# Kernel tuning notes

Measured on AMD Instinct MI355X. Metric: run time of the kernel, lower is better.

Reference implementation:

```python
import jax, jax.numpy as jnp
import numpy as np

C = 256          # channels
D = C // 4       # q/k dim and angle-embedding hidden_dim
SIGMA = 15.0
BN_EPS = 1e-5
N_LAYERS = 4


def angle_embed(angles, proj_w, proj_b):
    """AngleEmbedding: sinusoidal PE (detached in torch) + Linear proj.
    angles [...,], returns [..., D]. Interleaved sin/cos matches the torch
    cat([sin,cos],dim=2).view(...) layout."""
    factor = 180.0 / (np.pi * SIGMA)
    idx = angles * factor
    div_term = jnp.exp(jnp.arange(0, D, 2, dtype=jnp.float32) * (-np.log(10000.0) / D))  # [D/2]
    om = idx[..., None] * div_term                                  # [..., D/2]
    emb = jnp.stack([jnp.sin(om), jnp.cos(om)], axis=-1).reshape(*angles.shape, D)
    emb = jax.lax.stop_gradient(emb)  # torch: embeddings.detach()
    return emb @ proj_w.T + proj_b


def sa_layer(x, pca, a_self, a_cross, Wq, Wk, Wv, Wvp, Wl, bl, bn_g, bn_b,
             p1w, p1b, p2w, p2b, beta_x, beta_w, picked):
    # x, pca: [B, C, N]
    xq = jnp.einsum('oc,bcn->bno', Wq, x)              # [B,N,D]  q_conv (tied to k_conv_pca)
    k_lrf = jnp.einsum('oc,bcn->bon', Wk, x)           # [B,D,N]
    k_pca = jnp.einsum('oc,bcn->bon', Wq, pca)         # [B,D,N]  weight-tied to q
    energy_lrf = jnp.einsum('bno,bom->bnm', xq, k_lrf)
    energy_pca = jnp.einsum('bno,bom->bnm', xq, k_pca)
    # relative-angle bias terms
    emb1 = angle_embed(a_self, p1w, p1b)               # [B,N,N,D]
    energy_lrf = energy_lrf + jnp.einsum('bnc,bnmc->bnm', xq, emb1)
    emb2 = angle_embed(a_cross, p2w, p2b)              # [B,N,D]
    energy_pca = energy_pca + jnp.einsum('bnc,bmc->bnm', xq, emb2)
    # learn_weight=True combination, softmax over last dim, then column renorm
    energy = jax.nn.softmax(beta_w * energy_lrf + (1.0 - beta_w) * energy_pca, axis=-1)
    energy = energy / (1e-12 + energy.sum(axis=1, keepdims=True))
    point_relation = energy[:, picked, :][:, None, :]  # [B,1,N]
    x_lrf = jnp.einsum('oc,bcn,bnm->bom', Wv, x, energy)
    x_pca = jnp.einsum('oc,bcn,bnm->bom', Wvp, pca, energy)
    x_r = beta_x * x_lrf + (1.0 - beta_x) * x_pca
    h = jnp.einsum('oc,bcn->bon', Wl, x - x_r) + bl[:, None]
    # BatchNorm1d in eval mode: running_mean=0, running_var=1
    h = h / jnp.sqrt(1.0 + BN_EPS) * bn_g[:, None] + bn_b[:, None]
    return x + jax.nn.gelu(h, approximate=False), point_relation


def forward(lrf, pca, angle_self, angle_cross, Wq, Wk, Wv, Wvp, Wl, bl,
            bn_g, bn_b, p1w, p1b, p2w, p2b, beta_x, beta_w, picked):
    x = lrf
    outs = []
    for i in range(N_LAYERS):
        x, _ = sa_layer(x, pca, angle_self, angle_cross, Wq[i], Wk[i], Wv[i],
                        Wvp[i], Wl[i], bl[i], bn_g[i], bn_b[i], p1w[i], p1b[i],
                        p2w[i], p2b[i], beta_x[i], beta_w[i], picked)
        outs.append(x)
    return jnp.concatenate(outs, axis=1)   # [B, 4*C, N]


def setup_inputs() -> dict:
    key = jax.random.key(0)
    ks = jax.random.split(key, 18)
    B, N, L = 64, 128, N_LAYERS
    s = 0.05
    return {
        'lrf': jax.random.normal(ks[0], (B, C, N), dtype=jnp.float32),
        'pca': jax.random.normal(ks[1], (B, C, N), dtype=jnp.float32),
        'angle_self': jax.random.uniform(ks[2], (B, N, N), dtype=jnp.float32),
        'angle_cross': jax.random.uniform(ks[3], (B, N), dtype=jnp.float32),
        'Wq': jax.random.normal(ks[4], (L, D, C)) * s,
        'Wk': jax.random.normal(ks[5], (L, D, C)) * s,
        'Wv': jax.random.normal(ks[6], (L, C, C)) * s,
        'Wvp': jax.random.normal(ks[7], (L, C, C)) * s,
        'Wl': jax.random.normal(ks[8], (L, C, C)) * s,
        'bl': jax.random.normal(ks[9], (L, C)) * s,
        'bn_g': jnp.ones((L, C), dtype=jnp.float32),
        'bn_b': jnp.zeros((L, C), dtype=jnp.float32),
        'p1w': jax.random.normal(ks[10], (L, D, D)) * s,
        'p1b': jax.random.normal(ks[11], (L, D)) * s,
        'p2w': jax.random.normal(ks[12], (L, D, D)) * s,
        'p2b': jax.random.normal(ks[13], (L, D)) * s,
        'beta_x': jnp.full((L,), 0.6, dtype=jnp.float32),
        'beta_w': jnp.full((L,), 0.6, dtype=jnp.float32),
        'picked': 0,
    }


def reference(lrf, pca, angle_self, angle_cross, Wq, Wk, Wv, Wvp, Wl, bl,
              bn_g, bn_b, p1w, p1b, p2w, p2b, beta_x, beta_w, picked):
    return forward(lrf, pca, angle_self, angle_cross, Wq, Wk, Wv, Wvp, Wl, bl,
                   bn_g, bn_b, p1w, p1b, p2w, p2b, beta_x, beta_w, picked)
```

## Files before the change

kernel.cpp:

```cpp
#include <hip/hip_runtime.h>
#include <cstdint>
#include <cstddef>


#define BB 64
#define CH 256
#define NP 128
#define DQ 64
#define NLAYERS 4

#define ANG_FACTOR 3.8197186342054885f
#define DIV_STEP   0.28782313662425575f

#define LROW 264
#define LROW2 136

typedef unsigned short u16;
typedef __attribute__((ext_vector_type(8))) short sh8;
typedef __attribute__((ext_vector_type(4))) float f32x4;
#define MFMA(a, b, c) __builtin_amdgcn_mfma_f32_16x16x32_bf16(a, b, c, 0, 0, 0)

static __device__ __forceinline__ u16 f2bf(float x) {
  unsigned u = __float_as_uint(x);
  return (u16)((u + 0x7FFFu + ((u >> 16) & 1u)) >> 16);
}
static __device__ __forceinline__ float bf2f(u16 h) {
  return __uint_as_float(((unsigned)h) << 16);
}

__global__ __launch_bounds__(256) void k_init(
    const float* __restrict__ Wv, const float* __restrict__ Wvp,
    const float* __restrict__ Wl, const float* __restrict__ Wq,
    const float* __restrict__ Wk, const float* __restrict__ p1w,
    const float* __restrict__ p2w, const float* __restrict__ pca,
    const float* __restrict__ lrf, const float* __restrict__ ac,
    u16* __restrict__ Wlbf, u16* __restrict__ Wqhi, u16* __restrict__ Wqlo,
    u16* __restrict__ Wkhi, u16* __restrict__ Wklo, u16* __restrict__ p1wT,
    u16* __restrict__ p2wbf, u16* __restrict__ pThi, u16* __restrict__ pTlo,
    u16* __restrict__ xThi, u16* __restrict__ xTlo,
    u16* __restrict__ WvT, u16* __restrict__ WvpT, u16* __restrict__ emb2bf)
{
  __shared__ __align__(16) float tl[64 * 65];
  int blk = blockIdx.x, tid = threadIdx.x;
  if (blk < 256) {
    int i = (blk * 256 + tid) * 4;
    float4 v = *(const float4*)(Wl + i);
    u16 o[4] = {f2bf(v.x), f2bf(v.y), f2bf(v.z), f2bf(v.w)};
    *(uint2*)(Wlbf + i) = *(const uint2*)o;
  } else if (blk < 384) {
    int bb = blk - 256;
    const float* s = (bb < 64) ? Wq : Wk;
    u16* dh = (bb < 64) ? Wqhi : Wkhi;
    u16* dl = (bb < 64) ? Wqlo : Wklo;
    int i = ((bb & 63) * 256 + tid) * 4;
    float4 v = *(const float4*)(s + i);
    float vv[4] = {v.x, v.y, v.z, v.w};
    u16 h[4], l[4];
#pragma unroll
    for (int r = 0; r < 4; r++) {
      h[r] = f2bf(vv[r]);
      l[r] = f2bf(vv[r] - bf2f(h[r]));
    }
    *(uint2*)(dh + i) = *(const uint2*)h;
    *(uint2*)(dl + i) = *(const uint2*)l;
  } else if (blk < 388) {
    int l = blk - 384;
    const float* src = p1w + (size_t)l * DQ * DQ;
    u16* dst = p1wT + (size_t)l * DQ * DQ;
#pragma unroll
    for (int i = 0; i < 16; i++) {
      int idx = tid + i * 256;
      int dd = idx >> 6, oo = idx & 63;
      dst[idx] = f2bf(src[oo * DQ + dd]);
    }
  } else if (blk < 392) {
    int l = blk - 388;
    const float* src = p2w + (size_t)l * DQ * DQ;
    u16* dst = p2wbf + (size_t)l * DQ * DQ;
#pragma unroll
    for (int i = 0; i < 16; i++) {
      int idx = tid + i * 256;
      dst[idx] = f2bf(src[idx]);
    }
  } else if (blk < 1416) {
    int bi = blk - 392;
    int nt = bi & 1, y = (bi >> 1) & 7, b = bi >> 4;
    int ct = y & 3, is_lrf = y >> 2;
    const float* x = is_lrf ? lrf : pca;
    u16* hiT = is_lrf ? xThi : pThi;
    u16* loT = is_lrf ? xTlo : pTlo;
    {
      int col = tid & 63, rq = tid >> 6;
      const float* src = x + (size_t)b * CH * NP + (size_t)(ct * 64) * NP + nt * 64;
#pragma unroll
      for (int i = 0; i < 16; i++) {
        int c = rq + i * 4;
        tl[col * 65 + c] = src[(size_t)c * NP + col];
      }
// ... 119 lines not shown
    u16* WH = WS;
    u16* WL = WS + 32 * LROW;
    {
      const u16* sH = Wqhi + (size_t)l * DQ * CH + (size_t)dt * 32 * CH;
      const u16* sL = Wqlo + (size_t)l * DQ * CH + (size_t)dt * 32 * CH;
      STAGE_W(WH, sH)
      STAGE_W(WL, sL)
    }
    __syncthreads();
    const u16* B0h = pThi + ((size_t)b * NP + nt * 32 + lm) * CH + lk * 8;
    const u16* B1h = B0h + 16 * CH;
    const u16* B0l = pTlo + ((size_t)b * NP + nt * 32 + lm) * CH + lk * 8;
    const u16* B1l = B0l + 16 * CH;
    f32x4 acc[2][2] = {};
#pragma unroll
    for (int kb = 0; kb < 4; kb++) {
      sh8 rb0h[2], rb1h[2], rb0l[2], rb1l[2];
#pragma unroll
      for (int u = 0; u < 2; u++) {
        int o = (kb * 2 + u) * 32;
        rb0h[u] = *(const sh8*)(B0h + o); rb1h[u] = *(const sh8*)(B1h + o);
        rb0l[u] = *(const sh8*)(B0l + o); rb1l[u] = *(const sh8*)(B1l + o);
      }
#pragma unroll
      for (int u = 0; u < 2; u++) {
        int o2 = (kb * 2 + u) * 32 + lk * 8;
        sh8 a0h = *(const sh8*)&WH[lm * LROW + o2];
        sh8 a1h = *(const sh8*)&WH[(16 + lm) * LROW + o2];
        sh8 a0l = *(const sh8*)&WL[lm * LROW + o2];
        sh8 a1l = *(const sh8*)&WL[(16 + lm) * LROW + o2];
        acc[0][0] = MFMA(a0h, rb0h[u], acc[0][0]);
        acc[0][0] = MFMA(a0h, rb0l[u], acc[0][0]);
        acc[0][0] = MFMA(a0l, rb0h[u], acc[0][0]);
        acc[0][1] = MFMA(a0h, rb1h[u], acc[0][1]);
        acc[0][1] = MFMA(a0h, rb1l[u], acc[0][1]);
        acc[0][1] = MFMA(a0l, rb1h[u], acc[0][1]);
        acc[1][0] = MFMA(a1h, rb0h[u], acc[1][0]);
        acc[1][0] = MFMA(a1h, rb0l[u], acc[1][0]);
        acc[1][0] = MFMA(a1l, rb0h[u], acc[1][0]);
        acc[1][1] = MFMA(a1h, rb1h[u], acc[1][1]);
        acc[1][1] = MFMA(a1h, rb1l[u], acc[1][1]);
        acc[1][1] = MFMA(a1l, rb1h[u], acc[1][1]);
      }
    }
    {
      const u16* A20 = p2wbf + (size_t)l * DQ * DQ + ((size_t)(dt * 32) + lm) * DQ + lk * 8;
      const u16* A21 = A20 + 16 * DQ;
      const u16* B20 = emb2bf + ((size_t)b * NP + nt * 32 + lm) * DQ + lk * 8;
      const u16* B21 = B20 + 16 * DQ;
#pragma unroll
      for (int ks = 0; ks < 2; ks++) {
        int o = ks * 32;
        sh8 a0 = *(const sh8*)(A20 + o), a1 = *(const sh8*)(A21 + o);
        sh8 b0 = *(const sh8*)(B20 + o), b1 = *(const sh8*)(B21 + o);
        acc[0][0] = MFMA(a0, b0, acc[0][0]);
        acc[0][1] = MFMA(a0, b1, acc[0][1]);
        acc[1][0] = MFMA(a1, b0, acc[1][0]);
        acc[1][1] = MFMA(a1, b1, acc[1][1]);
      }
    }
#pragma unroll
    for (int i = 0; i < 2; i++)
#pragma unroll
      for (int j = 0; j < 2; j++) {
        int n = nt * 32 + j * 16 + lm;
        int d0 = dt * 32 + i * 16 + lk * 4;
        size_t off = (((size_t)l * BB + b) * NP + n) * DQ + d0;
        f32x4 v = acc[i][j];
        u16 h[4], lo[4];
#pragma unroll
        for (int r2 = 0; r2 < 4; r2++) {
          float vv = v[r2] + p2b[l * DQ + d0 + r2];
          h[r2] = f2bf(vv);
          lo[r2] = f2bf(vv - bf2f(h[r2]));
        }
        *(uint2*)&KP2hiA[off] = *(const uint2*)h;
        *(uint2*)&KP2loA[off] = *(const uint2*)lo;
      }
  } else {
    int bi = blockIdx.x - 512;
    int l = bi >> 9, rest = bi & 511;
    int ct = rest >> 6, b = rest & 63;
    int nt = tid >> 6;
    u16* WH = WS;
    {
      const u16* sH = M2b + (size_t)l * CH * CH + (size_t)ct * 32 * CH;
      STAGE_W(WH, sH)
    }
    __syncthreads();
    const u16* X0 = pThi + ((size_t)b * NP + nt * 32 + lm) * CH + lk * 8;
    const u16* X1 = X0 + 16 * CH;
    f32x4 a00 = {}, a01 = {}, a10 = {}, a11 = {};
#pragma unroll
    for (int kb = 0; kb < 2; kb++) {
      sh8 rx0[4], rx1[4];
#pragma unroll
      for (int u = 0; u < 4; u++) {
        int o = (kb * 4 + u) * 32;
        rx0[u] = *(const sh8*)(X0 + o); rx1[u] = *(const sh8*)(X1 + o);
      }
#pragma unroll
      for (int u = 0; u < 4; u++) {
        int o2 = (kb * 4 + u) * 32 + lk * 8;
        sh8 w0 = *(const sh8*)&WH[lm * LROW + o2];
        sh8 w1 = *(const sh8*)&WH[(16 + lm) * LROW + o2];
        a00 = MFMA(rx0[u], w0, a00);
        a01 = MFMA(rx0[u], w1, a01);
        a10 = MFMA(rx1[u], w0, a10);
        a11 = MFMA(rx1[u], w1, a11);
      }
    }
    f32x4 acc[2][2] = {{a00, a01}, {a10, a11}};
#pragma unroll
    for (int i = 0; i < 2; i++)
#pragma unroll
      for (int j = 0; j < 2; j++) {
        int n0 = nt * 32 + i * 16 + lk * 4;
        int c = ct * 32 + j * 16 + lm;
        u16 ov[4];
#pragma unroll
        for (int r2 = 0; r2 < 4; r2++) ov[r2] = f2bf(acc[i][j][r2]);
        *(uint2*)&WlUPA[(((size_t)l * BB + b) * CH + c) * NP + n0] = *(const uint2*)ov;
      }
  }
}

__global__ __launch_bounds__(256) void k_qu4(
    const u16* __restrict__ xThi, const u16* __restrict__ xTlo,
    const u16* __restrict__ Wqhi, const u16* __restrict__ Wqlo,
    const u16* __restrict__ Wkhi, const u16* __restrict__ Wklo,
    const u16* __restrict__ Mb, const u16* __restrict__ Wlbf,
    const u16* __restrict__ WlUP, u16* __restrict__ XQhi, u16* __restrict__ XQlo,
    u16* __restrict__ KLThi, u16* __restrict__ KLTlo,
    u16* __restrict__ WlU, float* __restrict__ Afp)
{
  __shared__ __align__(16) u16 WS[2 * 32 * LROW];
  int tid = threadIdx.x, lane = tid & 63;
  int lm = lane & 15, lk = lane >> 4;
  if (blockIdx.x < 256) {
    int bi = blockIdx.x;
    int mat = bi >> 7, rest = bi & 127;
    int dt = rest >> 6, b = rest & 63;
    int nt = tid >> 6;
    u16* WH = WS;
    u16* WL = WS + 32 * LROW;
    {
      const u16* sH = (mat ? Wkhi : Wqhi) + (size_t)dt * 32 * CH;
      const u16* sL = (mat ? Wklo : Wqlo) + (size_t)dt * 32 * CH;
      STAGE_W(WH, sH)
      STAGE_W(WL, sL)
    }
    __syncthreads();
    const u16* B0h = xThi + ((size_t)b * NP + nt * 32 + lm) * CH + lk * 8;
    const u16* B1h = B0h + 16 * CH;
    const u16* B0l = xTlo + ((size_t)b * NP + nt * 32 + lm) * CH + lk * 8;
    const u16* B1l = B0l + 16 * CH;
    f32x4 acc[2][2] = {};
#pragma unroll
    for (int kb = 0; kb < 4; kb++) {
      sh8 rb0h[2], rb1h[2], rb0l[2], rb1l[2];
#pragma unroll
      for (int u = 0; u < 2; u++) {
        int o = (kb * 2 + u) * 32;
        rb0h[u] = *(const sh8*)(B0h + o); rb1h[u] = *(const sh8*)(B1h + o);
        rb0l[u] = *(const sh8*)(B0l + o); rb1l[u] = *(const sh8*)(B1l + o);
      }
#pragma unroll
      for (int u = 0; u < 2; u++) {
        int o2 = (kb * 2 + u) * 32 + lk * 8;
        sh8 a0h = *(const sh8*)&WH[lm * LROW + o2];
        sh8 a1h = *(const sh8*)&WH[(16 + lm) * LROW + o2];
        sh8 a0l = *(const sh8*)&WL[lm * LROW + o2];
        sh8 a1l = *(const sh8*)&WL[(16 + lm) * LROW + o2];
        acc[0][0] = MFMA(a0h, rb0h[u], acc[0][0]);
        acc[0][0] = MFMA(a0h, rb0l[u], acc[0][0]);
        acc[0][0] = MFMA(a0l, rb0h[u], acc[0][0]);
        acc[0][1] = MFMA(a0h, rb1h[u], acc[0][1]);
        acc[0][1] = MFMA(a0h, rb1l[u], acc[0][1]);
        acc[0][1] = MFMA(a0l, rb1h[u], acc[0][1]);
        acc[1][0] = MFMA(a1h, rb0h[u], acc[1][0]);
        acc[1][0] = MFMA(a1h, rb0l[u], acc[1][0]);
        acc[1][0] = MFMA(a1l, rb0h[u], acc[1][0]);
        acc[1][1] = MFMA(a1h, rb1h[u], acc[1][1]);
        acc[1][1] = MFMA(a1h, rb1l[u], acc[1][1]);
        acc[1][1] = MFMA(a1l, rb1h[u], acc[1][1]);
      }
    }
#pragma unroll
    for (int i = 0; i < 2; i++)
#pragma unroll
      for (int j = 0; j < 2; j++) {
        int n = nt * 32 + j * 16 + lm;
        int d0 = dt * 32 + i * 16 + lk * 4;
        size_t off = ((size_t)b * NP + n) * DQ + d0;
        f32x4 v = acc[i][j];
        u16 h[4], lo[4];
#pragma unroll
        for (int r2 = 0; r2 < 4; r2++) {
          h[r2] = f2bf(v[r2]);
          lo[r2] = f2bf(v[r2] - bf2f(h[r2]));
        }
        if (mat == 0) {
          *(uint2*)&XQhi[off] = *(const uint2*)h;
          *(uint2*)&XQlo[off] = *(const uint2*)lo;
        } else {
          *(uint2*)&KLThi[off] = *(const uint2*)h;
          *(uint2*)&KLTlo[off] = *(const uint2*)lo;
        }
      }
  } else if (blockIdx.x < 768) {
    int bi = blockIdx.x - 256;
    int ct = bi >> 6, b = bi & 63;
    int nt = tid >> 6;
    u16* WH = WS;
    {
      const u16* sH = Mb + (size_t)ct * 32 * CH;
      STAGE_W(WH, sH)
    }
    __syncthreads();
    const u16* X0 = xThi + ((size_t)b * NP + nt * 32 + lm) * CH + lk * 8;
    const u16* X1 = X0 + 16 * CH;
    f32x4 a00 = {}, a01 = {}, a10 = {}, a11 = {};
#pragma unroll
    for (int kb = 0; kb < 2; kb++) {
      sh8 rx0[4], rx1[4];
#pragma unroll
      for (int u = 0; u < 4; u++) {
        int o = (kb * 4 + u) * 32;
        rx0[u] = *(const sh8*)(X0 + o); rx1[u] = *(const sh8*)(X1 + o);
      }
#pragma unroll
      for (int u = 0; u < 4; u++) {
        int o2 = (kb * 4 + u) * 32 + lk * 8;
        sh8 w0 = *(const sh8*)&WH[lm * LROW + o2];
        sh8 w1 = *(const sh8*)&WH[(16 + lm) * LROW + o2];
        a00 = MFMA(rx0[u], w0, a00);
        a01 = MFMA(rx0[u], w1, a01);
        a10 = MFMA(rx1[u], w0, a10);
        a11 = MFMA(rx1[u], w1, a11);
      }
    }
    f32x4 acc[2][2] = {{a00, a01}, {a10, a11}};
#pragma unroll
    for (int i = 0; i < 2; i++)
#pragma unroll
      for (int j = 0; j < 2; j++) {
        int n0 = nt * 32 + i * 16 + lk * 4;
        int c = ct * 32 + j * 16 + lm;
        size_t off = ((size_t)b * CH + c) * NP + n0;
        uint2 up = *(const uint2*)&WlUP[off];
        const u16* uph = (const u16*)&up;
        u16 ov[4];
#pragma unroll
        for (int r2 = 0; r2 < 4; r2++)
          ov[r2] = f2bf(acc[i][j][r2] + bf2f(uph[r2]));
        *(uint2*)&WlU[off] = *(const uint2*)ov;
      }
  } else {
    int bi = blockIdx.x - 768;
    int ct = bi >> 6, b = bi & 63;
    int nt = tid >> 6;
    u16* WH = WS;
    {
      const u16* sH = Wlbf + (size_t)ct * 32 * CH;
      STAGE_W(WH, sH)
    }
    __syncthreads();
    const u16* X0 = xThi + ((size_t)b * NP + nt * 32 + lm) * CH + lk * 8;
    const u16* X1 = X0 + 16 * CH;
    f32x4 a00 = {}, a01 = {}, a10 = {}, a11 = {};
#pragma unroll
    for (int kb = 0; kb < 2; kb++) {
      sh8 rx0[4], rx1[4];
#pragma unroll
      for (int u = 0; u < 4; u++) {
        int o = (kb * 4 + u) * 32;
        rx0[u] = *(const sh8*)(X0 + o); rx1[u] = *(const sh8*)(X1 + o);
      }
#pragma unroll
      for (int u = 0; u < 4; u++) {
        int o2 = (kb * 4 + u) * 32 + lk * 8;
        sh8 w0 = *(const sh8*)&WH[lm * LROW + o2];
        sh8 w1 = *(const sh8*)&WH[(16 + lm) * LROW + o2];
        a00 = MFMA(rx0[u], w0, a00);
        a01 = MFMA(rx0[u], w1, a01);
        a10 = MFMA(rx1[u], w0, a10);
        a11 = MFMA(rx1[u], w1, a11);
      }
    }
    f32x4 acc[2][2] = {{a00, a01}, {a10, a11}};
#pragma unroll
    for (int i = 0; i < 2; i++)
#pragma unroll
      for (int j = 0; j < 2; j++) {
        int n0 = nt * 32 + i * 16 + lk * 4;
        int c = ct * 32 + j * 16 + lm;
        float4 v = {acc[i][j][0], acc[i][j][1], acc[i][j][2], acc[i][j][3]};
        *(float4*)&Afp[((size_t)b * CH + c) * NP + n0] = v;
      }
  }
}

__global__ __launch_bounds__(256) void k_att(
    const u16* __restrict__ XQhi, const u16* __restrict__ XQlo,
    const u16* __restrict__ KLThi, const u16* __restrict__ KLTlo,
    const u16* __restrict__ KP2hi, const u16* __restrict__ KP2lo,
    const u16* __restrict__ p1wT, const float* __restrict__ p1b,
    const float* __restrict__ AS, const float* __restrict__ beta_w, int layer,
    u16* __restrict__ PT, float* __restrict__ SCLp)
{
  __shared__ __align__(16) char smem[25856];
  int tid = threadIdx.x;
  int lane = tid & 63;
  int lm = lane & 15, lk = lane >> 4;
  int g = blockIdx.x & 3, b = blockIdx.x >> 2;
  int wave = tid >> 6;
  float* q1sh = (float*)smem;
  float* c1sh = q1sh + 32 * 66;
  float* divs = c1sh + 32;
  float* Esh  = divs + 32;
  if (tid < 32) divs[tid] = __expf(-(float)tid * DIV_STEP);
  float bw = beta_w[layer], obw = 1.0f - bw;
  {
    int mt = wave;
    size_t arow = ((size_t)b * NP + mt * 32 + lm) * DQ + lk * 8;
    size_t brow = ((size_t)b * NP + g * 32 + lm) * DQ + lk * 8;
    const u16* L0h = KLThi + arow;
    const u16* L0l = KLTlo + arow;
    const u16* P0h = KP2hi + arow;
    const u16* P0l = KP2lo + arow;
    const u16* X0h = XQhi + brow;
    const u16* X0l = XQlo + brow;
    sh8 xh[2][2], xl[2][2], lh[2][2], llr[2][2], ph[2][2], pl[2][2];
#pragma unroll
    for (int row = 0; row < 2; row++) {
#pragma unroll
      for (int ks = 0; ks < 2; ks++) {
        int o = row * 16 * DQ + ks * 32;
        xh[row][ks] = *(const sh8*)(X0h + o);
        xl[row][ks] = *(const sh8*)(X0l + o);
        lh[row][ks] = *(const sh8*)(L0h + o);
        llr[row][ks] = *(const sh8*)(L0l + o);
        ph[row][ks] = *(const sh8*)(P0h + o);
        pl[row][ks] = *(const sh8*)(P0l + o);
      }
    }
    f32x4 aL[2][2] = {};
    f32x4 aP[2][2] = {};
#pragma unroll
    for (int ks = 0; ks < 2; ks++) {
#pragma unroll
      for (int i = 0; i < 2; i++) {
#pragma unroll
        for (int j = 0; j < 2; j++) {
          aL[i][j] = MFMA(lh[i][ks], xh[j][ks], aL[i][j]);
          aL[i][j] = MFMA(lh[i][ks], xl[j][ks], aL[i][j]);
          aL[i][j] = MFMA(llr[i][ks], xh[j][ks], aL[i][j]);
          aP[i][j] = MFMA(ph[i][ks], xh[j][ks], aP[i][j]);
          aP[i][j] = MFMA(ph[i][ks], xl[j][ks], aP[i][j]);
          aP[i][j] = MFMA(pl[i][ks], xh[j][ks], aP[i][j]);
        }
      }
    }
#pragma unroll
    for (int i = 0; i < 2; i++)
#pragma unroll
      for (int j = 0; j < 2; j++) {
        int nloc = j * 16 + lm;
        int mloc = mt * 32 + i * 16 + lk * 4;
        float4 v;
        v.x = bw * aL[i][j][0] + obw * aP[i][j][0];
        v.y = bw * aL[i][j][1] + obw * aP[i][j][1];
        v.z = bw * aL[i][j][2] + obw * aP[i][j][2];
        v.w = bw * aL[i][j][3] + obw * aP[i][j][3];
        *(float4*)&Esh[nloc * 132 + mloc] = v;
      }
  }
  if (wave < 2) {
    const u16* A0 = XQhi + ((size_t)b * NP + g * 32 + lm) * DQ + lk * 8;
    const u16* A1 = A0 + 16 * DQ;
    const u16* B0 = p1wT + ((size_t)(wave * 32) + lm) * DQ + lk * 8;
    const u16* B1 = B0 + 16 * DQ;
    f32x4 q[2][2] = {};
// ... 20 lines not shown
    const u16* xs = XQhi + ((size_t)b * NP + g * 32 + n) * DQ + o0;
    uint2 w0 = *(const uint2*)xs;
    uint2 w1 = *(const uint2*)(xs + 4);
    const u16* hh = (const u16*)&w0;
    const u16* h2 = (const u16*)&w1;
    float s = 0.0f;
#pragma unroll
    for (int k = 0; k < 4; k++) s = fmaf(bf2f(hh[k]), p1b[o0 + k], s);
#pragma unroll
    for (int k = 0; k < 4; k++) s = fmaf(bf2f(h2[k]), p1b[o0 + 4 + k], s);
    s += __shfl_xor(s, 1);
    s += __shfl_xor(s, 2);
    s += __shfl_xor(s, 4);
    if ((tid & 7) == 0) c1sh[n] = s;
  }
  __syncthreads();
  {
    int n = tid >> 3, mc = (tid & 7) * 16;
    size_t asrow = ((size_t)b * NP + g * 32 + n) * NP + mc;
    float idxv[16], bias[16];
    float c1v = c1sh[n];
#pragma unroll
    for (int k4 = 0; k4 < 4; k4++) {
      float4 a4 = *(const float4*)&AS[asrow + k4 * 4];
      idxv[k4 * 4 + 0] = a4.x * ANG_FACTOR;
      idxv[k4 * 4 + 1] = a4.y * ANG_FACTOR;
      idxv[k4 * 4 + 2] = a4.z * ANG_FACTOR;
      idxv[k4 * 4 + 3] = a4.w * ANG_FACTOR;
    }
#pragma unroll
    for (int k = 0; k < 16; k++) bias[k] = c1v;
    for (int j = 0; j < 32; j++) {
      float dv = divs[j];
      float qs = q1sh[n * 66 + 2 * j], qc = q1sh[n * 66 + 2 * j + 1];
#pragma unroll
      for (int k = 0; k < 16; k++) {
        float s, c;
        __sincosf(idxv[k] * dv, &s, &c);
        bias[k] = fmaf(qs, s, bias[k]);
        bias[k] = fmaf(qc, c, bias[k]);
      }
    }
    float ev[16], mx = -1e30f;
#pragma unroll
    for (int k = 0; k < 16; k++) {
      ev[k] = Esh[n * 132 + mc + k] + bw * bias[k];
      mx = fmaxf(mx, ev[k]);
    }
    mx = fmaxf(mx, __shfl_xor(mx, 1));
    mx = fmaxf(mx, __shfl_xor(mx, 2));
    mx = fmaxf(mx, __shfl_xor(mx, 4));
    float s = 0.0f;
#pragma unroll
    for (int k = 0; k < 16; k++) {
      ev[k] = __expf(ev[k] - mx);
      s += ev[k];
    }
    s += __shfl_xor(s, 1);
    s += __shfl_xor(s, 2);
    s += __shfl_xor(s, 4);
    float inv = 1.0f / s;
#pragma unroll
    for (int k = 0; k < 16; k++) Esh[n * 132 + mc + k] = ev[k] * inv;
  }
  __syncthreads();
  {
    int m = tid >> 1, nc = (tid & 1) * 16;
    float s = 0.0f;
    u16 tmp[16];
#pragma unroll
    for (int k = 0; k < 16; k++) {
      float v = Esh[(nc + k) * 132 + m];
      s += v;
      tmp[k] = f2bf(v);
    }
    u16* dst = PT + ((size_t)b * NP + m) * NP + g * 32 + nc;
    *(uint4*)&dst[0] = *(const uint4*)&tmp[0];
    *(uint4*)&dst[8] = *(const uint4*)&tmp[8];
    s += __shfl_xor(s, 1);
    if ((tid & 1) == 0) SCLp[((size_t)b * 4 + g) * NP + m] = s;
  }
}

__global__ __launch_bounds__(256) void k_h3(
    const u16* __restrict__ WlU, const u16* __restrict__ PT,
    const float* __restrict__ SCLp, const float* __restrict__ Afp,
    const float* __restrict__ bl, const float* __restrict__ bng,
    const float* __restrict__ bnb, const float* __restrict__ xsrc, int xbs,
    float* __restrict__ out, int layer,
    u16* __restrict__ xThi_o, u16* __restrict__ xTlo_o)
{
  int bi = blockIdx.x;
  int ct = bi >> 6, b = bi & 63;
  int tid = threadIdx.x, lane = tid & 63, nt = tid >> 6;
  int lm = lane & 15, lk = lane >> 4;
  __shared__ __align__(16) u16 WS2[32 * LROW2];
  {
    const u16* src = WlU + ((size_t)b * CH + ct * 32) * NP;
#pragma unroll
    for (int it = 0; it < 2; it++) {
      int idx = tid + it * 256, row = idx >> 4, chq = idx & 15;
      *(uint4*)&WS2[row * LROW2 + chq * 8] = *(const uint4*)(src + row * NP + chq * 8);
    }
  }
  __syncthreads();
  const u16* B0 = PT + ((size_t)b * NP + nt * 32 + lm) * NP + lk * 8;
  const u16* B1 = B0 + 16 * NP;
  sh8 rB0[4], rB1[4];
#pragma unroll
  for (int ks = 0; ks < 4; ks++) {
    int o = ks * 32;
    rB0[ks] = *(const sh8*)(B0 + o);
    rB1[ks] = *(const sh8*)(B1 + o);
  }
  f32x4 a00 = {}, a01 = {}, a10 = {}, a11 = {};
#pragma unroll
  for (int ks = 0; ks < 4; ks++) {
    int o2 = ks * 32 + lk * 8;
    sh8 w0 = *(const sh8*)&WS2[lm * LROW2 + o2];
    sh8 w1 = *(const sh8*)&WS2[(16 + lm) * LROW2 + o2];
    a00 = MFMA(w0, rB0[ks], a00);
    a01 = MFMA(w0, rB1[ks], a01);
    a10 = MFMA(w1, rB0[ks], a10);
    a11 = MFMA(w1, rB1[ks], a11);
  }
  f32x4 acc[2][2] = {{a00, a01}, {a10, a11}};
  const float rbn = 0.999995000037499687f;
#pragma unroll
  for (int i = 0; i < 2; i++)
#pragma unroll
    for (int j = 0; j < 2; j++) {
      int m = nt * 32 + j * 16 + lm;
      int cq = ct * 32 + i * 16 + lk * 4;
      const float* sp = SCLp + (size_t)b * 4 * NP + m;
      float scl = 1.0f / (1e-12f + sp[0] + sp[NP] + sp[2 * NP] + sp[3 * NP]);
      u16 hh[4], llv[4];
#pragma unroll
      for (int r = 0; r < 4; r++) {
        int c = cq + r;
        float a = Afp[((size_t)b * CH + c) * NP + m];
        float h = a - acc[i][j][r] * scl + bl[c];
        h = h * rbn * bng[c] + bnb[c];
        float gg = 0.5f * h * (1.0f + erff(h * 0.70710678118654752440f));
        float ov = xsrc[(size_t)b * xbs + (size_t)c * NP + m] + gg;
        out[((size_t)b * 4 * CH + (size_t)layer * CH + c) * NP + m] = ov;
        hh[r] = f2bf(ov);
        llv[r] = f2bf(ov - bf2f(hh[r]));
      }
      size_t xoff = ((size_t)b * NP + m) * CH + cq;
      *(uint2*)&xThi_o[xoff] = *(const uint2*)hh;
      *(uint2*)&xTlo_o[xoff] = *(const uint2*)llv;
    }
}

extern "C" void kernel_launch(void* const* d_in, const int* in_sizes, int n_in,
                              void* d_out, int out_size, void* d_ws, size_t ws_size,
                              hipStream_t stream)
{
  (void)in_sizes; (void)n_in; (void)out_size; (void)ws_size;
  const float* lrf     = (const float*)d_in[0];
  const float* pca     = (const float*)d_in[1];
  const float* a_self  = (const float*)d_in[2];
  const float* a_cross = (const float*)d_in[3];
  const float* Wq  = (const float*)d_in[4];
  const float* Wk  = (const float*)d_in[5];
  const float* Wv  = (const float*)d_in[6];
  const float* Wvp = (const float*)d_in[7];
  const float* Wl  = (const float*)d_in[8];
  const float* bl  = (const float*)d_in[9];
  const float* bng = (const float*)d_in[10];
  const float* bnb = (const float*)d_in[11];
  const float* p1w = (const float*)d_in[12];
  const float* p1b = (const float*)d_in[13];
  const float* p2w = (const float*)d_in[14];
  const float* p2b = (const float*)d_in[15];
  const float* beta_x = (const float*)d_in[16];
  const float* beta_w = (const float*)d_in[17];
  float* out = (float*)d_out;
  float* ws  = (float*)d_ws;

  const size_t QKN = (size_t)BB * NP * DQ;
  const size_t ENN = (size_t)BB * NP * NP;
  const size_t XCN = (size_t)BB * NP * CH;

  float* SCLp = ws;
  float* Afp  = SCLp + (size_t)BB * 4 * NP;
  u16* up = (u16*)(Afp + (size_t)BB * CH * NP);
  u16* xThi = up;   up += XCN;
  u16* xTlo = up;   up += XCN;
  u16* pThi = up;   up += XCN;
  u16* pTlo = up;   up += XCN;
  u16* XQhi = up;   up += QKN;
  u16* XQlo = up;   up += QKN;
  u16* KLThi = up;  up += QKN;
  u16* KLTlo = up;  up += QKN;
  u16* KP2hiA = up; up += (size_t)NLAYERS * QKN;
  u16* KP2loA = up; up += (size_t)NLAYERS * QKN;
  u16* WlUPA = up;  up += (size_t)NLAYERS * XCN;
  u16* WlUb = up;   up += XCN;
  u16* PTbf = up;   up += ENN;
  u16* Wlbf = up;   up += (size_t)NLAYERS * CH * CH;
  u16* WvT = up;    up += (size_t)NLAYERS * CH * CH;
  u16* WvpT = up;   up += (size_t)NLAYERS * CH * CH;
  u16* Mb = up;     up += (size_t)NLAYERS * CH * CH;
  u16* M2b = up;    up += (size_t)NLAYERS * CH * CH;
  u16* Wqhi = up;   up += (size_t)NLAYERS * DQ * CH;
  u16* Wqlo = up;   up += (size_t)NLAYERS * DQ * CH;
  u16* Wkhi = up;   up += (size_t)NLAYERS * DQ * CH;
  u16* Wklo = up;   up += (size_t)NLAYERS * DQ * CH;
  u16* p1wT = up;   up += (size_t)NLAYERS * DQ * DQ;
  u16* p2wbf = up;  up += (size_t)NLAYERS * DQ * DQ;
  u16* emb2bf = up; up += QKN;

  k_init<<<dim3(2568), 256, 0, stream>>>(
      Wv, Wvp, Wl, Wq, Wk, p1w, p2w, pca, lrf, a_cross,
      Wlbf, Wqhi, Wqlo, Wkhi, Wklo, p1wT, p2wbf,
      pThi, pTlo, xThi, xTlo, WvT, WvpT, emb2bf);
  k_mm<<<dim3(128), 256, 0, stream>>>(WvT, WvpT, Wlbf, beta_x, Mb, M2b);
  k_pre2<<<dim3(2560), 256, 0, stream>>>(
      pThi, pTlo, Wqhi, Wqlo, M2b, p2wbf, emb2bf, p2b,
      KP2hiA, KP2loA, WlUPA);

  for (int l = 0; l < NLAYERS; l++) {
    const float* xsrc = (l == 0) ? lrf : (out + (size_t)(l - 1) * CH * NP);
    int xbs = (l == 0) ? CH * NP : 4 * CH * NP;
    k_qu4<<<dim3(1280), 256, 0, stream>>>(
        xThi, xTlo,
        Wqhi + (size_t)l * DQ * CH, Wqlo + (size_t)l * DQ * CH,
        Wkhi + (size_t)l * DQ * CH, Wklo + (size_t)l * DQ * CH,
        Mb + (size_t)l * CH * CH, Wlbf + (size_t)l * CH * CH,
        WlUPA + (size_t)l * XCN,
        XQhi, XQlo, KLThi, KLTlo, WlUb, Afp);
    k_att<<<dim3(256), 256, 0, stream>>>(
        XQhi, XQlo, KLThi, KLTlo,
        KP2hiA + (size_t)l * QKN, KP2loA + (size_t)l * QKN,
        p1wT + (size_t)l * DQ * DQ, p1b + (size_t)l * DQ,
        a_self, beta_w, l, PTbf, SCLp);
    k_h3<<<dim3(512), 256, 0, stream>>>(
        WlUb, PTbf, SCLp, Afp, bl + (size_t)l * CH, bng + (size_t)l * CH,
        bnb + (size_t)l * CH, xsrc, xbs, out, l, xThi, xTlo);
  }
}
```

Measured before the change: 239.0 us.

## Fuse Mb/Wl projections into final h kernel, double-buffer x bf16 inputs

```diff
diff --git a/kernel.cpp b/kernel.cpp
--- a/kernel.cpp
+++ b/kernel.cpp
@@ -13,7 +13,6 @@
 #define DIV_STEP   0.28782313662425575f
 
 #define LROW 264
-#define LROW2 136
 
 typedef unsigned short u16;
 typedef __attribute__((ext_vector_type(8))) short sh8;
@@ -299,10 +298,9 @@
     int l = bi >> 9, rest = bi & 511;
     int ct = rest >> 6, b = rest & 63;
     int nt = tid >> 6;
-    u16* WH = WS;
     {
       const u16* sH = M2b + (size_t)l * CH * CH + (size_t)ct * 32 * CH;
-      STAGE_W(WH, sH)
+      STAGE_W(WS, sH)
     }
     __syncthreads();
     const u16* X0 = pThi + ((size_t)b * NP + nt * 32 + lm) * CH + lk * 8;
@@ -319,12 +317,12 @@
 #pragma unroll
       for (int u = 0; u < 4; u++) {
         int o2 = (kb * 4 + u) * 32 + lk * 8;
-        sh8 w0 = *(const sh8*)&WH[lm * LROW + o2];
-        sh8 w1 = *(const sh8*)&WH[(16 + lm) * LROW + o2];
-        a00 = MFMA(rx0[u], w0, a00);
-        a01 = MFMA(rx0[u], w1, a01);
-        a10 = MFMA(rx1[u], w0, a10);
-        a11 = MFMA(rx1[u], w1, a11);
+        sh8 w0 = *(const sh8*)&WS[lm * LROW + o2];
+        sh8 w1 = *(const sh8*)&WS[(16 + lm) * LROW + o2];
+        a00 = MFMA(w0, rx0[u], a00);
+        a01 = MFMA(w0, rx1[u], a01);
+        a10 = MFMA(w1, rx0[u], a10);
+        a11 = MFMA(w1, rx1[u], a11);
       }
     }
     f32x4 acc[2][2] = {{a00, a01}, {a10, a11}};
@@ -332,190 +330,96 @@
     for (int i = 0; i < 2; i++)
 #pragma unroll
       for (int j = 0; j < 2; j++) {
-        int n0 = nt * 32 + i * 16 + lk * 4;
-        int c = ct * 32 + j * 16 + lm;
+        int c0 = ct * 32 + i * 16 + lk * 4;
+        int n = nt * 32 + j * 16 + lm;
         u16 ov[4];
 #pragma unroll
         for (int r2 = 0; r2 < 4; r2++) ov[r2] = f2bf(acc[i][j][r2]);
-        *(uint2*)&WlUPA[(((size_t)l * BB + b) * CH + c) * NP + n0] = *(const uint2*)ov;
+        *(uint2*)&WlUPA[(((size_t)l * BB + b) * NP + n) * CH + c0] = *(const uint2*)ov;
       }
   }
 }
 
-__global__ __launch_bounds__(256) void k_qu4(
+__global__ __launch_bounds__(256) void k_qk(
     const u16* __restrict__ xThi, const u16* __restrict__ xTlo,
     const u16* __restrict__ Wqhi, const u16* __restrict__ Wqlo,
     const u16* __restrict__ Wkhi, const u16* __restrict__ Wklo,
-    const u16* __restrict__ Mb, const u16* __restrict__ Wlbf,
-    const u16* __restrict__ WlUP, u16* __restrict__ XQhi, u16* __restrict__ XQlo,
-    u16* __restrict__ KLThi, u16* __restrict__ KLTlo,
-    u16* __restrict__ WlU, float* __restrict__ Afp)
+    u16* __restrict__ XQhi, u16* __restrict__ XQlo,
+    u16* __restrict__ KLThi, u16* __restrict__ KLTlo)
 {
   __shared__ __align__(16) u16 WS[2 * 32 * LROW];
   int tid = threadIdx.x, lane = tid & 63;
   int lm = lane & 15, lk = lane >> 4;
-  if (blockIdx.x < 256) {
-    int bi = blockIdx.x;
-    int mat = bi >> 7, rest = bi & 127;
-    int dt = rest >> 6, b = rest & 63;
-    int nt = tid >> 6;
-    u16* WH = WS;
-    u16* WL = WS + 32 * LROW;
-    {
-      const u16* sH = (mat ? Wkhi : Wqhi) + (size_t)dt * 32 * CH;
-      const u16* sL = (mat ? Wklo : Wqlo) + (size_t)dt * 32 * CH;
-      STAGE_W(WH, sH)
-      STAGE_W(WL, sL)
-    }
-    __syncthreads();
-    const u16* B0h = xThi + ((size_t)b * NP + nt * 32 + lm) * CH + lk * 8;
-    const u16* B1h = B0h + 16 * CH;
-    const u16* B0l = xTlo + ((size_t)b * NP + nt * 32 + lm) * CH + lk * 8;
-    const u16* B1l = B0l + 16 * CH;
-    f32x4 acc[2][2] = {};
-#pragma unroll
-    for (int kb = 0; kb < 4; kb++) {
-      sh8 rb0h[2], rb1h[2], rb0l[2], rb1l[2];
-#pragma unroll
-      for (int u = 0; u < 2; u++) {
-        int o = (kb * 2 + u) * 32;
-        rb0h[u] = *(const sh8*)(B0h + o); rb1h[u] = *(const sh8*)(B1h + o);
-        rb0l[u] = *(const sh8*)(B0l + o); rb1l[u] = *(const sh8*)(B1l + o);
-      }
-#pragma unroll
-      for (int u = 0; u < 2; u++) {
-        int o2 = (kb * 2 + u) * 32 + lk * 8;
-        sh8 a0h = *(const sh8*)&WH[lm * LROW + o2];
-        sh8 a1h = *(const sh8*)&WH[(16 + lm) * LROW + o2];
-        sh8 a0l = *(const sh8*)&WL[lm * LROW + o2];
-        sh8 a1l = *(const sh8*)&WL[(16 + lm) * LROW + o2];
-        acc[0][0] = MFMA(a0h, rb0h[u], acc[0][0]);
-        acc[0][0] = MFMA(a0h, rb0l[u], acc[0][0]);
-        acc[0][0] = MFMA(a0l, rb0h[u], acc[0][0]);
-        acc[0][1] = MFMA(a0h, rb1h[u], acc[0][1]);
-        acc[0][1] = MFMA(a0h, rb1l[u], acc[0][1]);
-        acc[0][1] = MFMA(a0l, rb1h[u], acc[0][1]);
-        acc[1][0] = MFMA(a1h, rb0h[u], acc[1][0]);
-        acc[1][0] = MFMA(a1h, rb0l[u], acc[1][0]);
-        acc[1][0] = MFMA(a1l, rb0h[u], acc[1][0]);
-        acc[1][1] = MFMA(a1h, rb1h[u], acc[1][1]);
-        acc[1][1] = MFMA(a1h, rb1l[u], acc[1][1]);
-        acc[1][1] = MFMA(a1l, rb1h[u], acc[1][1]);
-      }
-    }
-#pragma unroll
-    for (int i = 0; i < 2; i++)
-#pragma unroll
-      for (int j = 0; j < 2; j++) {
-        int n = nt * 32 + j * 16 + lm;
-        int d0 = dt * 32 + i * 16 + lk * 4;
-        size_t off = ((size_t)b * NP + n) * DQ + d0;
-        f32x4 v = acc[i][j];
-        u16 h[4], lo[4];
-#pragma unroll
-        for (int r2 = 0; r2 < 4; r2++) {
-          h[r2] = f2bf(v[r2]);
-          lo[r2] = f2bf(v[r2] - bf2f(h[r2]));
-        }
-        if (mat == 0) {
-          *(uint2*)&XQhi[off] = *(const uint2*)h;
-          *(uint2*)&XQlo[off] = *(const uint2*)lo;
-        } else {
-          *(uint2*)&KLThi[off] = *(const uint2*)h;
-          *(uint2*)&KLTlo[off] = *(const uint2*)lo;
-        }
-      }
-  } else if (blockIdx.x < 768) {
-    int bi = blockIdx.x - 256;
-    int ct = bi >> 6, b = bi & 63;
-    int nt = tid >> 6;
-    u16* WH = WS;
-    {
-      const u16* sH = Mb + (size_t)ct * 32 * CH;
-      STAGE_W(WH, sH)
-    }
-    __syncthreads();
-    const u16* X0 = xThi + ((size_t)b * NP + nt * 32 + lm) * CH + lk * 8;
-    const u16* X1 = X0 + 16 * CH;
-    f32x4 a00 = {}, a01 = {}, a10 = {}, a11 = {};
-#pragma unroll
-    for (int kb = 0; kb < 2; kb++) {
-      sh8 rx0[4], rx1[4];
-#pragma unroll
-      for (int u = 0; u < 4; u++) {
-        int o = (kb * 4 + u) * 32;
-        rx0[u] = *(const sh8*)(X0 + o); rx1[u] = *(const sh8*)(X1 + o);
-      }
-#pragma unroll
-      for (int u = 0; u < 4; u++) {
-        int o2 = (kb * 4 + u) * 32 + lk * 8;
-        sh8 w0 = *(const sh8*)&WH[lm * LROW + o2];
-        sh8 w1 = *(const sh8*)&WH[(16 + lm) * LROW + o2];
-        a00 = MFMA(rx0[u], w0, a00);
-        a01 = MFMA(rx0[u], w1, a01);
-        a10 = MFMA(rx1[u], w0, a10);
-        a11 = MFMA(rx1[u], w1, a11);
-      }
-    }
-    f32x4 acc[2][2] = {{a00, a01}, {a10, a11}};
-#pragma unroll
-    for (int i = 0; i < 2; i++)
-#pragma unroll
-      for (int j = 0; j < 2; j++) {
-        int n0 = nt * 32 + i * 16 + lk * 4;
-        int c = ct * 32 + j * 16 + lm;
-        size_t off = ((size_t)b * CH + c) * NP + n0;
-        uint2 up = *(const uint2*)&WlUP[off];
-        const u16* uph = (const u16*)&up;
-        u16 ov[4];
-#pragma unroll
-        for (int r2 = 0; r2 < 4; r2++)
-          ov[r2] = f2bf(acc[i][j][r2] + bf2f(uph[r2]));
-        *(uint2*)&WlU[off] = *(const uint2*)ov;
-      }
-  } else {
-    int bi = blockIdx.x - 768;
-    int ct = bi >> 6, b = bi & 63;
-    int nt = tid >> 6;
-    u16* WH = WS;
-    {
-      const u16* sH = Wlbf + (size_t)ct * 32 * CH;
-      STAGE_W(WH, sH)
-    }
-    __syncthreads();
-    const u16* X0 = xThi + ((size_t)b * NP + nt * 32 + lm) * CH + lk * 8;
-    const u16* X1 = X0 + 16 * CH;
-    f32x4 a00 = {}, a01 = {}, a10 = {}, a11 = {};
-#pragma unroll
-    for (int kb = 0; kb < 2; kb++) {
-      sh8 rx0[4], rx1[4];
-#pragma unroll
-      for (int u = 0; u < 4; u++) {
-        int o = (kb * 4 + u) * 32;
-        rx0[u] = *(const sh8*)(X0 + o); rx1[u] = *(const sh8*)(X1 + o);
-      }
-#pragma unroll
-      for (int u = 0; u < 4; u++) {
-        int o2 = (kb * 4 + u) * 32 + lk * 8;
-        sh8 w0 = *(const sh8*)&WH[lm * LROW + o2];
-        sh8 w1 = *(const sh8*)&WH[(16 + lm) * LROW + o2];
-        a00 = MFMA(rx0[u], w0, a00);
-        a01 = MFMA(rx0[u], w1, a01);
-        a10 = MFMA(rx1[u], w0, a10);
-        a11 = MFMA(rx1[u], w1, a11);
-      }
-    }
-    f32x4 acc[2][2] = {{a00, a01}, {a10, a11}};
-#pragma unroll
-    for (int i = 0; i < 2; i++)
-#pragma unroll
-      for (int j = 0; j < 2; j++) {
-        int n0 = nt * 32 + i * 16 + lk * 4;
-        int c = ct * 32 + j * 16 + lm;
-        float4 v = {acc[i][j][0], acc[i][j][1], acc[i][j][2], acc[i][j][3]};
-        *(float4*)&Afp[((size_t)b * CH + c) * NP + n0] = v;
-      }
-  }
+  int bi = blockIdx.x;
+  int mat = bi >> 7, rest = bi & 127;
+  int dt = rest >> 6, b = rest & 63;
+  int nt = tid >> 6;
+  u16* WH = WS;
+  u16* WL = WS + 32 * LROW;
+  {
+    const u16* sH = (mat ? Wkhi : Wqhi) + (size_t)dt * 32 * CH;
+    const u16* sL = (mat ? Wklo : Wqlo) + (size_t)dt * 32 * CH;
+    STAGE_W(WH, sH)
+    STAGE_W(WL, sL)
+  }
+  __syncthreads();
+  const u16* B0h = xThi + ((size_t)b * NP + nt * 32 + lm) * CH + lk * 8;
+  const u16* B1h = B0h + 16 * CH;
+  const u16* B0l = xTlo + ((size_t)b * NP + nt * 32 + lm) * CH + lk * 8;
+  const u16* B1l = B0l + 16 * CH;
+  f32x4 acc[2][2] = {};
+#pragma unroll
+  for (int kb = 0; kb < 4; kb++) {
+    sh8 rb0h[2], rb1h[2], rb0l[2], rb1l[2];
+#pragma unroll
+    for (int u = 0; u < 2; u++) {
+      int o = (kb * 2 + u) * 32;
+      rb0h[u] = *(const sh8*)(B0h + o); rb1h[u] = *(const sh8*)(B1h + o);
+      rb0l[u] = *(const sh8*)(B0l + o); rb1l[u] = *(const sh8*)(B1l + o);
+    }
+#pragma unroll
+    for (int u = 0; u < 2; u++) {
+      int o2 = (kb * 2 + u) * 32 + lk * 8;
+      sh8 a0h = *(const sh8*)&WH[lm * LROW + o2];
+      sh8 a1h = *(const sh8*)&WH[(16 + lm) * LROW + o2];
+      sh8 a0l = *(const sh8*)&WL[lm * LROW + o2];
+      sh8 a1l = *(const sh8*)&WL[(16 + lm) * LROW + o2];
+      acc[0][0] = MFMA(a0h, rb0h[u], acc[0][0]);
+      acc[0][0] = MFMA(a0h, rb0l[u], acc[0][0]);
+      acc[0][0] = MFMA(a0l, rb0h[u], acc[0][0]);
+      acc[0][1] = MFMA(a0h, rb1h[u], acc[0][1]);
+      acc[0][1] = MFMA(a0h, rb1l[u], acc[0][1]);
+      acc[0][1] = MFMA(a0l, rb1h[u], acc[0][1]);
+      acc[1][0] = MFMA(a1h, rb0h[u], acc[1][0]);
+      acc[1][0] = MFMA(a1h, rb0l[u], acc[1][0]);
+      acc[1][0] = MFMA(a1l, rb0h[u], acc[1][0]);
+      acc[1][1] = MFMA(a1h, rb1h[u], acc[1][1]);
+      acc[1][1] = MFMA(a1h, rb1l[u], acc[1][1]);
+      acc[1][1] = MFMA(a1l, rb1h[u], acc[1][1]);
+    }
+  }
+#pragma unroll
+  for (int i = 0; i < 2; i++)
+#pragma unroll
+    for (int j = 0; j < 2; j++) {
+      int n = nt * 32 + j * 16 + lm;
+      int d0 = dt * 32 + i * 16 + lk * 4;
+      size_t off = ((size_t)b * NP + n) * DQ + d0;
+      f32x4 v = acc[i][j];
+      u16 h[4], lo[4];
+#pragma unroll
+      for (int r2 = 0; r2 < 4; r2++) {
+        h[r2] = f2bf(v[r2]);
+        lo[r2] = f2bf(v[r2] - bf2f(h[r2]));
+      }
+      if (mat == 0) {
+        *(uint2*)&XQhi[off] = *(const uint2*)h;
+        *(uint2*)&XQlo[off] = *(const uint2*)lo;
+      } else {
+        *(uint2*)&KLThi[off] = *(const uint2*)h;
+        *(uint2*)&KLTlo[off] = *(const uint2*)lo;
+      }
+    }
 }
 
 __global__ __launch_bounds__(256) void k_att(
@@ -702,55 +606,95 @@
   }
 }
 
-__global__ __launch_bounds__(256) void k_h3(
-    const u16* __restrict__ WlU, const u16* __restrict__ PT,
-    const float* __restrict__ SCLp, const float* __restrict__ Afp,
+__global__ __launch_bounds__(256) void k_h4(
+    const u16* __restrict__ xThi, const u16* __restrict__ Mb,
+    const u16* __restrict__ Wlbf, const u16* __restrict__ WlUP,
+    const u16* __restrict__ PT, const float* __restrict__ SCLp,
     const float* __restrict__ bl, const float* __restrict__ bng,
     const float* __restrict__ bnb, const float* __restrict__ xsrc, int xbs,
     float* __restrict__ out, int layer,
     u16* __restrict__ xThi_o, u16* __restrict__ xTlo_o)
 {
-  int bi = blockIdx.x;
-  int ct = bi >> 6, b = bi & 63;
-  int tid = threadIdx.x, lane = tid & 63, nt = tid >> 6;
+  __shared__ __align__(16) u16 WS[2 * 32 * LROW];
+  int ct = blockIdx.x >> 6, b = blockIdx.x & 63;
+  int tid = threadIdx.x, lane = tid & 63, wave = tid >> 6;
   int lm = lane & 15, lk = lane >> 4;
-  __shared__ __align__(16) u16 WS2[32 * LROW2];
+  u16* MT = WS;
+  u16* WT = WS + 32 * LROW;
   {
-    const u16* src = WlU + ((size_t)b * CH + ct * 32) * NP;
-#pragma unroll
-    for (int it = 0; it < 2; it++) {
-      int idx = tid + it * 256, row = idx >> 4, chq = idx & 15;
-      *(uint4*)&WS2[row * LROW2 + chq * 8] = *(const uint4*)(src + row * NP + chq * 8);
-    }
+    const u16* sM = Mb + (size_t)ct * 32 * CH;
+    const u16* sW = Wlbf + (size_t)ct * 32 * CH;
+    STAGE_W(MT, sM)
+    STAGE_W(WT, sW)
   }
   __syncthreads();
-  const u16* B0 = PT + ((size_t)b * NP + nt * 32 + lm) * NP + lk * 8;
+  const u16* X0 = xThi + ((size_t)b * NP + wave * 32 + lm) * CH + lk * 8;
+  const u16* X1 = X0 + 16 * CH;
+  f32x4 awl[2][2] = {};
+  f32x4 afp[2][2] = {};
+#pragma unroll
+  for (int kb = 0; kb < 2; kb++) {
+    sh8 rx0[4], rx1[4];
+#pragma unroll
+    for (int u = 0; u < 4; u++) {
+      int o = (kb * 4 + u) * 32;
+      rx0[u] = *(const sh8*)(X0 + o);
+      rx1[u] = *(const sh8*)(X1 + o);
+    }
+#pragma unroll
+    for (int u = 0; u < 4; u++) {
+      int o2 = (kb * 4 + u) * 32 + lk * 8;
+      sh8 m0 = *(const sh8*)&MT[lm * LROW + o2];
+      sh8 m1 = *(const sh8*)&MT[(16 + lm) * LROW + o2];
+      sh8 w0 = *(const sh8*)&WT[lm * LROW + o2];
+      sh8 w1 = *(const sh8*)&WT[(16 + lm) * LROW + o2];
+      awl[0][0] = MFMA(m0, rx0[u], awl[0][0]);
+      awl[0][1] = MFMA(m0, rx1[u], awl[0][1]);
+      awl[1][0] = MFMA(m1, rx0[u], awl[1][0]);
+      awl[1][1] = MFMA(m1, rx1[u], awl[1][1]);
+      afp[0][0] = MFMA(w0, rx0[u], afp[0][0]);
+      afp[0][1] = MFMA(w0, rx1[u], afp[0][1]);
+      afp[1][0] = MFMA(w1, rx0[u], afp[1][0]);
+      afp[1][1] = MFMA(w1, rx1[u], afp[1][1]);
+    }
+  }
+  __syncthreads();
+  u16* wluS = WS;
+#pragma unroll
+  for (int i = 0; i < 2; i++)
+#pragma unroll
+    for (int j = 0; j < 2; j++) {
+      int cl = i * 16 + lk * 4;
+      int n = wave * 32 + j * 16 + lm;
+      uint2 up = *(const uint2*)&WlUP[((size_t)b * NP + n) * CH + ct * 32 + cl];
+      const u16* uph = (const u16*)&up;
+#pragma unroll
+      for (int r = 0; r < 4; r++)
+        wluS[(cl + r) * 136 + n] = f2bf(awl[i][j][r] + bf2f(uph[r]));
+    }
+  __syncthreads();
+  const u16* B0 = PT + ((size_t)b * NP + wave * 32 + lm) * NP + lk * 8;
   const u16* B1 = B0 + 16 * NP;
-  sh8 rB0[4], rB1[4];
+  f32x4 acc2[2][2] = {};
 #pragma unroll
   for (int ks = 0; ks < 4; ks++) {
     int o = ks * 32;
-    rB0[ks] = *(const sh8*)(B0 + o);
-    rB1[ks] = *(const sh8*)(B1 + o);
-  }
-  f32x4 a00 = {}, a01 = {}, a10 = {}, a11 = {};
-#pragma unroll
-  for (int ks = 0; ks < 4; ks++) {
+    sh8 b0 = *(const sh8*)(B0 + o);
+    sh8 b1 = *(const sh8*)(B1 + o);
     int o2 = ks * 32 + lk * 8;
-    sh8 w0 = *(const sh8*)&WS2[lm * LROW2 + o2];
-    sh8 w1 = *(const sh8*)&WS2[(16 + lm) * LROW2 + o2];
-    a00 = MFMA(w0, rB0[ks], a00);
-    a01 = MFMA(w0, rB1[ks], a01);
-    a10 = MFMA(w1, rB0[ks], a10);
-    a11 = MFMA(w1, rB1[ks], a11);
-  }
-  f32x4 acc[2][2] = {{a00, a01}, {a10, a11}};
+    sh8 a0 = *(const sh8*)&wluS[lm * 136 + o2];
+    sh8 a1 = *(const sh8*)&wluS[(16 + lm) * 136 + o2];
+    acc2[0][0] = MFMA(a0, b0, acc2[0][0]);
+    acc2[0][1] = MFMA(a0, b1, acc2[0][1]);
+    acc2[1][0] = MFMA(a1, b0, acc2[1][0]);
+    acc2[1][1] = MFMA(a1, b1, acc2[1][1]);
+  }
   const float rbn = 0.999995000037499687f;
 #pragma unroll
   for (int i = 0; i < 2; i++)
 #pragma unroll
     for (int j = 0; j < 2; j++) {
-      int m = nt * 32 + j * 16 + lm;
+      int m = wave * 32 + j * 16 + lm;
       int cq = ct * 32 + i * 16 + lk * 4;
       const float* sp = SCLp + (size_t)b * 4 * NP + m;
       float scl = 1.0f / (1e-12f + sp[0] + sp[NP] + sp[2 * NP] + sp[3 * NP]);
@@ -758,8 +702,7 @@
 #pragma unroll
       for (int r = 0; r < 4; r++) {
         int c = cq + r;
-        float a = Afp[((size_t)b * CH + c) * NP + m];
-        float h = a - acc[i][j][r] * scl + bl[c];
+        float h = afp[i][j][r] - acc2[i][j][r] * scl + bl[c];
         h = h * rbn * bng[c] + bnb[c];
         float gg = 0.5f * h * (1.0f + erff(h * 0.70710678118654752440f));
         float ov = xsrc[(size_t)b * xbs + (size_t)c * NP + m] + gg;
@@ -804,10 +747,11 @@
   const size_t XCN = (size_t)BB * NP * CH;
 
   float* SCLp = ws;
-  float* Afp  = SCLp + (size_t)BB * 4 * NP;
-  u16* up = (u16*)(Afp + (size_t)BB * CH * NP);
-  u16* xThi = up;   up += XCN;
-  u16* xTlo = up;   up += XCN;
+  u16* up = (u16*)(SCLp + (size_t)BB * 4 * NP);
+  u16* xThiA = up;  up += XCN;
+  u16* xTloA = up;  up += XCN;
+  u16* xThiB = up;  up += XCN;
+  u16* xTloB = up;  up += XCN;
   u16* pThi = up;   up += XCN;
   u16* pTlo = up;   up += XCN;
   u16* XQhi = up;   up += QKN;
@@ -817,7 +761,6 @@
   u16* KP2hiA = up; up += (size_t)NLAYERS * QKN;
   u16* KP2loA = up; up += (size_t)NLAYERS * QKN;
   u16* WlUPA = up;  up += (size_t)NLAYERS * XCN;
-  u16* WlUb = up;   up += XCN;
   u16* PTbf = up;   up += ENN;
   u16* Wlbf = up;   up += (size_t)NLAYERS * CH * CH;
   u16* WvT = up;    up += (size_t)NLAYERS * CH * CH;
@@ -835,7 +778,7 @@
   k_init<<<dim3(2568), 256, 0, stream>>>(
       Wv, Wvp, Wl, Wq, Wk, p1w, p2w, pca, lrf, a_cross,
       Wlbf, Wqhi, Wqlo, Wkhi, Wklo, p1wT, p2wbf,
-      pThi, pTlo, xThi, xTlo, WvT, WvpT, emb2bf);
+      pThi, pTlo, xThiA, xTloA, WvT, WvpT, emb2bf);
   k_mm<<<dim3(128), 256, 0, stream>>>(WvT, WvpT, Wlbf, beta_x, Mb, M2b);
   k_pre2<<<dim3(2560), 256, 0, stream>>>(
       pThi, pTlo, Wqhi, Wqlo, M2b, p2wbf, emb2bf, p2b,
@@ -844,20 +787,24 @@
   for (int l = 0; l < NLAYERS; l++) {
     const float* xsrc = (l == 0) ? lrf : (out + (size_t)(l - 1) * CH * NP);
     int xbs = (l == 0) ? CH * NP : 4 * CH * NP;
-    k_qu4<<<dim3(1280), 256, 0, stream>>>(
-        xThi, xTlo,
+    u16* xhi_in  = (l & 1) ? xThiB : xThiA;
+    u16* xlo_in  = (l & 1) ? xTloB : xTloA;
+    u16* xhi_out = (l & 1) ? xThiA : xThiB;
+    u16* xlo_out = (l & 1) ? xTloA : xTloB;
+    k_qk<<<dim3(256), 256, 0, stream>>>(
+        xhi_in, xlo_in,
         Wqhi + (size_t)l * DQ * CH, Wqlo + (size_t)l * DQ * CH,
         Wkhi + (size_t)l * DQ * CH, Wklo + (size_t)l * DQ * CH,
-        Mb + (size_t)l * CH * CH, Wlbf + (size_t)l * CH * CH,
-        WlUPA + (size_t)l * XCN,
-        XQhi, XQlo, KLThi, KLTlo, WlUb, Afp);
+        XQhi, XQlo, KLThi, KLTlo);
     k_att<<<dim3(256), 256, 0, stream>>>(
         XQhi, XQlo, KLThi, KLTlo,
         KP2hiA + (size_t)l * QKN, KP2loA + (size_t)l * QKN,
         p1wT + (size_t)l * DQ * DQ, p1b + (size_t)l * DQ,
         a_self, beta_w, l, PTbf, SCLp);
-    k_h3<<<dim3(512), 256, 0, stream>>>(
-        WlUb, PTbf, SCLp, Afp, bl + (size_t)l * CH, bng + (size_t)l * CH,
-        bnb + (size_t)l * CH, xsrc, xbs, out, l, xThi, xTlo);
+    k_h4<<<dim3(512), 256, 0, stream>>>(
+        xhi_in, Mb + (size_t)l * CH * CH, Wlbf + (size_t)l * CH * CH,
+        WlUPA + (size_t)l * XCN, PTbf, SCLp,
+        bl + (size_t)l * CH, bng + (size_t)l * CH, bnb + (size_t)l * CH,
+        xsrc, xbs, out, l, xhi_out, xlo_out);
   }
 }
```

Measured after the change: 207.5 us. 1.15x faster.
